# Optimization experiments

Measured on AMD Instinct MI355X. Metric: run time of the kernel, lower is better.

The kernel has to match this reference:

```python
import jax, jax.numpy as jnp
import numpy as np

V = 327696       # total nodes (4 graphs x 2 hemis x 40962 verts)
E = 1966080      # directed edges
C = 64           # feature dim
G = 4            # num graphs (subjects)
EPS = 1e-5


def setup_inputs() -> dict:
    key = jax.random.key(0)
    ks = jax.random.split(key, 10)
    x = jax.random.normal(ks[0], (V, C), dtype=jnp.float32)
    edge_index = jax.random.randint(ks[1], (2, E), 0, V, dtype=jnp.int64)
    batch = jnp.sort(jax.random.randint(ks[2], (V,), 0, G, dtype=jnp.int64))
    s = 1.0 / np.sqrt(C)
    return {
        "x": x,
        "edge_index": edge_index,
        "batch": batch,
        # GraphNorm 1 (PyG init: weight=1, bias=0, mean_scale=1)
        "norm1_w": jnp.ones((C,), jnp.float32),
        "norm1_b": jnp.zeros((C,), jnp.float32),
        "norm1_ms": jnp.ones((C,), jnp.float32),
        # SAGEConv linear layers: lin_l (on max-aggregated neighbors, with bias), lin_r (root, no bias)
        "lin_l_w": jax.random.uniform(ks[3], (C, C), jnp.float32, -s, s),
        "lin_l_b": jax.random.uniform(ks[4], (C,), jnp.float32, -s, s),
        "lin_r_w": jax.random.uniform(ks[5], (C, C), jnp.float32, -s, s),
        # GraphNorm 2
        "norm2_w": jnp.ones((C,), jnp.float32),
        "norm2_b": jnp.zeros((C,), jnp.float32),
        "norm2_ms": jnp.ones((C,), jnp.float32),
    }


def graph_norm(x, batch, weight, bias, mean_scale):
    # per-graph mean/var over nodes (PyG GraphNorm)
    ones = jnp.ones((x.shape[0], 1), x.dtype)
    cnt = jax.ops.segment_sum(ones, batch, num_segments=G)            # [G,1]
    mean = jax.ops.segment_sum(x, batch, num_segments=G) / cnt       # [G,C]
    centered = x - mean[batch] * mean_scale
    var = jax.ops.segment_sum(centered * centered, batch, num_segments=G) / cnt
    inv_std = jax.lax.rsqrt(var + EPS)
    return weight * centered * inv_std[batch] + bias


def sage_conv_max(x, edge_index, lin_l_w, lin_l_b, lin_r_w):
    src, dst = edge_index[0], edge_index[1]
    # scatter-max of source features onto destinations (irregular access)
    agg = jax.ops.segment_max(x[src], dst, num_segments=V)
    agg = jnp.where(jnp.isneginf(agg), 0.0, agg)  # nodes with no in-edges -> 0
    return agg @ lin_l_w + lin_l_b + x @ lin_r_w


def reference(x, edge_index, batch, norm1_w, norm1_b, norm1_ms,
              lin_l_w, lin_l_b, lin_r_w, norm2_w, norm2_b, norm2_ms):
    h = graph_norm(x, batch, norm1_w, norm1_b, norm1_ms)
    h = sage_conv_max(h, edge_index, lin_l_w, lin_l_b, lin_r_w)
    h = jax.nn.relu(x + h)
    h = graph_norm(h, batch, norm2_w, norm2_b, norm2_ms)
    return h
```

## Files before the change

kernel.cpp:

```cpp
#include <hip/hip_runtime.h>

#define V_NODES 327696
#define E_EDGES 1966080
#define C_DIM   64
#define G_NUM   4
#define EPS_GN  1e-5f
#define N_TILES (V_NODES/16)
#define SAGE_BLOCKS 2048
#define WAVES_TOTAL (SAGE_BLOCKS*4)
#define FILL_BLOCKS 512
#define H_BLOCKS 2048
#define NB_SCAN 1281
#define CH_SCAN2 6
#define PW 520
#define STAT_BLOCKS 2048
#define STAT_WAVES (STAT_BLOCKS*4)
#define TOTAL_F4 (V_NODES*16)
#define SW_CHUNK 640
#define HIST_BLOCKS 960

typedef short bf16x8 __attribute__((ext_vector_type(8)));
typedef float f32x4  __attribute__((ext_vector_type(4)));
typedef unsigned uintx4 __attribute__((ext_vector_type(4)));
typedef int intx4 __attribute__((ext_vector_type(4)));
typedef unsigned short u16x2 __attribute__((ext_vector_type(2)));

__device__ __forceinline__ unsigned short f2bf(float f) {
    unsigned u = __float_as_uint(f);
    return (unsigned short)((u + 0x7FFFu + ((u >> 16) & 1u)) >> 16);
}
__device__ __forceinline__ unsigned short encbf(float f) {
    unsigned short b = f2bf(f);
    return b ^ (unsigned short)(0x8000u | ((b >> 15) * 0x7FFFu));
}
__device__ __forceinline__ unsigned decp(unsigned e) {
    unsigned s = e & 0x80008000u;
    unsigned m = (s >> 15) * 0x7FFFu;
    return e ^ ~m;
}
__device__ __forceinline__ unsigned pkmaxu(unsigned a, unsigned b) {
    u16x2 xa = __builtin_bit_cast(u16x2, a);
    u16x2 xb = __builtin_bit_cast(u16x2, b);
    u16x2 r  = __builtin_elementwise_max(xa, xb);
    return __builtin_bit_cast(unsigned, r);
}

__global__ __launch_bounds__(256) void k_stats(const float* __restrict__ x,
                                               const int* __restrict__ batch,
                                               float* __restrict__ partial1) {
    __shared__ float red_s[256], red_q[256], red_c[G_NUM];
    const int t = threadIdx.x;
    red_s[t] = 0.0f; red_q[t] = 0.0f;
    if (t < G_NUM) red_c[t] = 0.0f;
    __syncthreads();

    const int w    = blockIdx.x * 4 + (t >> 6);
    const int lane = t & 63;
    const int base = w * SW_CHUNK;
    const int end  = (w == STAT_WAVES - 1) ? TOTAL_F4 : base + SW_CHUNK;
    const int c4   = (lane & 15) << 2;
    const bool cntr = (lane & 15) == 0;
    const float4* x4p = (const float4*)x;

    const int g0 = batch[base >> 4];
    const int g1 = batch[(end - 1) >> 4];

    if (g0 == g1 && end == base + SW_CHUNK) {
        float4 su = {0,0,0,0}, qu = {0,0,0,0};
        #pragma unroll
        for (int it = 0; it < 10; it++) {
            float4 v = x4p[base + lane + it * 64];
            su.x += v.x; su.y += v.y; su.z += v.z; su.w += v.w;
            qu.x = fmaf(v.x, v.x, qu.x); qu.y = fmaf(v.y, v.y, qu.y);
            qu.z = fmaf(v.z, v.z, qu.z); qu.w = fmaf(v.w, v.w, qu.w);
        }
        int p = (g0 << 6) + c4;
        atomicAdd(&red_s[p],   su.x); atomicAdd(&red_q[p],   qu.x);
        atomicAdd(&red_s[p+1], su.y); atomicAdd(&red_q[p+1], qu.y);
        atomicAdd(&red_s[p+2], su.z); atomicAdd(&red_q[p+2], qu.z);
        atomicAdd(&red_s[p+3], su.w); atomicAdd(&red_q[p+3], qu.w);
        if (cntr) atomicAdd(&red_c[g0], 10.0f);
    } else {
        for (int idx = base + lane; idx < end; idx += 64) {
            float4 v = x4p[idx];
            int g = batch[idx >> 4];
            int p = (g << 6) + c4;
            atomicAdd(&red_s[p],   v.x); atomicAdd(&red_q[p],   v.x * v.x);
            atomicAdd(&red_s[p+1], v.y); atomicAdd(&red_q[p+1], v.y * v.y);
            atomicAdd(&red_s[p+2], v.z); atomicAdd(&red_q[p+2], v.z * v.z);
            atomicAdd(&red_s[p+3], v.w); atomicAdd(&red_q[p+3], v.w * v.w);
            if (cntr) atomicAdd(&red_c[g], 1.0f);
        }
    }
    __syncthreads();
    float* row = partial1 + (size_t)blockIdx.x * PW;
    row[t] = red_s[t]; row[256 + t] = red_q[t];
    if (t < G_NUM) row[512 + t] = red_c[t];
}

__global__ __launch_bounds__(256) void k_hist(const int* __restrict__ ei,
                                              int* __restrict__ hist,
                                              unsigned short* __restrict__ rank) {
    const int t = blockIdx.x * 256 + threadIdx.x;
    const int* dst = ei + E_EDGES;
    const int e0 = t * 4;
    const int e1 = (E_EDGES / 2) + t * 4;
    intx4 a = *(const intx4*)(dst + e0);
    intx4 b = *(const intx4*)(dst + e1);
    int r0 = atomicAdd(&hist[a[0]], 1);
    int r1 = atomicAdd(&hist[a[1]], 1);
    int r2 = atomicAdd(&hist[a[2]], 1);
    int r3 = atomicAdd(&hist[a[3]], 1);
    int r4 = atomicAdd(&hist[b[0]], 1);
    int r5 = atomicAdd(&hist[b[1]], 1);
    int r6 = atomicAdd(&hist[b[2]], 1);
    int r7 = atomicAdd(&hist[b[3]], 1);
    ushort4 wa = { (unsigned short)r0, (unsigned short)r1,
                   (unsigned short)r2, (unsigned short)r3 };
    ushort4 wb = { (unsigned short)r4, (unsigned short)r5,
                   (unsigned short)r6, (unsigned short)r7 };
    *(ushort4*)(rank + e0) = wa;
    *(ushort4*)(rank + e1) = wb;
}

__global__ __launch_bounds__(256) void k_red(const float* __restrict__ partial,
                                             int nblocks, int nent,
                                             float* __restrict__ outs,
                                             float* __restrict__ outc) {
    int e = blockIdx.x * 4 + (threadIdx.x >> 6);
    int lane = threadIdx.x & 63;
    if (e >= nent) return;
    float s = 0.0f;
    for (int b = lane; b < nblocks; b += 64) s += partial[(size_t)b * PW + e];
    #pragma unroll
    for (int off = 1; off < 64; off <<= 1) s += __shfl_xor(s, off);
    if (lane == 0) { if (e < 512) outs[e] = s; else outc[e - 512] = s; }
}

__global__ __launch_bounds__(256) void k_scan1(const int* __restrict__ hist,
                                               int* __restrict__ bsum) {
    __shared__ int s[256];
    int i = blockIdx.x * 256 + threadIdx.x;
    s[threadIdx.x] = (i < V_NODES) ? hist[i] : 0;
    __syncthreads();
    for (int off = 128; off > 0; off >>= 1) {
        if (threadIdx.x < off) s[threadIdx.x] += s[threadIdx.x + off];
        __syncthreads();
    }
    if (threadIdx.x == 0) bsum[blockIdx.x] = s[0];
}

__global__ __launch_bounds__(256) void k_params(const float* __restrict__ sum,
                                                const float* __restrict__ sumsq,
                                                const float* __restrict__ cnt,
                                                const float* __restrict__ w,
                                                const float* __restrict__ b,
                                                const float* __restrict__ ms,
                                                float* __restrict__ scale,
                                                float* __restrict__ shift,
                                                const float* __restrict__ Wl,
                                                const float* __restrict__ Wr,
                                                char* __restrict__ gWsw,
                                                int do_wt,
                                                int* __restrict__ bsum) {
    if (blockIdx.x == 0) {
        int t = threadIdx.x;
        int g = t >> 6, c = t & 63;
        float n    = cnt[g];
        float mean = sum[t] / n;
        float msq  = sumsq[t] / n;
        float m    = ms[c];
        float var  = msq - 2.0f*m*mean*mean + m*m*mean*mean;
        float inv  = rsqrtf(var + EPS_GN);
        float sc   = w[c] * inv;
        scale[t] = sc;
        shift[t] = b[c] - mean * m * sc;
        if (do_wt) {
            for (int i = threadIdx.x; i < C_DIM*C_DIM; i += 256) {
                int k = i >> 6, col = i & 63;
                int boff = (col*128 + k*2) ^ ((col & 7) << 4);
                *(unsigned short*)(gWsw + boff)        = f2bf(Wl[i]);
                *(unsigned short*)(gWsw + 8192 + boff) = f2bf(Wr[i]);
            }
        }
    } else {
        __shared__ int s[256];
        int t = threadIdx.x;
        int loc[CH_SCAN2];
        int mysum = 0;
        #pragma unroll
        for (int j = 0; j < CH_SCAN2; j++) {
            int idx = t * CH_SCAN2 + j;
            loc[j] = (idx < NB_SCAN) ? bsum[idx] : 0;
            mysum += loc[j];
        }
        s[t] = mysum;
        __syncthreads();
        for (int off = 1; off < 256; off <<= 1) {
            int tmp = (t >= off) ? s[t - off] : 0;
            __syncthreads();
            s[t] += tmp;
            __syncthreads();
        }
        int ex = s[t] - mysum;
        #pragma unroll
        for (int j = 0; j < CH_SCAN2; j++) {
            int idx = t * CH_SCAN2 + j;
            if (idx < NB_SCAN) { bsum[idx] = ex; ex += loc[j]; }
        }
    }
}

__global__ __launch_bounds__(256) void k_scan3(const int* __restrict__ hist,
                                               const int* __restrict__ bsum,
                                               int* __restrict__ offs) {
    __shared__ int s[256];
    int t = threadIdx.x;
    int i = blockIdx.x * 256 + t;
    int v = (i < V_NODES) ? hist[i] : 0;
    s[t] = v;
    __syncthreads();
    for (int off = 1; off < 256; off <<= 1) {
        int tmp = (t >= off) ? s[t - off] : 0;
        __syncthreads();
        s[t] += tmp;
        __syncthreads();
    }
    int ex = s[t] - v + bsum[blockIdx.x];
    if (i < V_NODES) offs[i] = ex;
    if (i == 0) offs[V_NODES] = E_EDGES;
}

__global__ __launch_bounds__(256) void k_h_fill(const float* __restrict__ x,
                                                const int* __restrict__ batch,
                                                const float* __restrict__ scale1,
                                                const float* __restrict__ shift1,
                                                unsigned short* __restrict__ henc,
                                                const int* __restrict__ ei,
                                                const unsigned short* __restrict__ rank,
                                                const int* __restrict__ offs,
                                                int* __restrict__ slots) {
    if (blockIdx.x < FILL_BLOCKS) {
        int stride = FILL_BLOCKS * 256;
        for (int e = blockIdx.x * 256 + threadIdx.x; e < E_EDGES; e += stride) {
            int src = ei[e];
            int d   = ei[E_EDGES + e];
            slots[offs[d] + (int)rank[e]] = src;
        }
        return;
    }
    __shared__ float sc[256], sh[256];
    sc[threadIdx.x] = scale1[threadIdx.x];
    sh[threadIdx.x] = shift1[threadIdx.x];
    __syncthreads();
    const int total = V_NODES * 16;
    int bid = blockIdx.x - FILL_BLOCKS;
    int stride = H_BLOCKS * 256;
    const float4* x4 = (const float4*)x;
    ushort4* h4 = (ushort4*)henc;
    for (int i = bid * 256 + threadIdx.x; i < total; i += stride) {
        int v  = i >> 4;
        int c4 = (i & 15) << 2;
        int g  = batch[v];
        int p  = (g << 6) | c4;
        float4 val = x4[i];
        ushort4 o;
        o.x = encbf(fmaf(val.x, sc[p],   sh[p]));
        o.y = encbf(fmaf(val.y, sc[p+1], sh[p+1]));
        o.z = encbf(fmaf(val.z, sc[p+2], sh[p+2]));
        o.w = encbf(fmaf(val.w, sc[p+3], sh[p+3]));
        h4[i] = o;
    }
}

__global__ __launch_bounds__(256) void k_sage(const unsigned short* __restrict__ henc,
                                              const float* __restrict__ x,
                                              const int* __restrict__ batch,
                                              const int* __restrict__ offs,
                                              const int* __restrict__ slots,
                                              const char* __restrict__ gWsw,
                                              const float* __restrict__ bl,
                                              float* __restrict__ out,
                                              float* __restrict__ partial2) {
    __shared__ char lds_w[16384];
    __shared__ float red_s[256], red_q[256];
    {
        const float4* wsrc = (const float4*)gWsw;
        float4* wdst = (float4*)lds_w;
        for (int t = threadIdx.x; t < 1024; t += 256) wdst[t] = wsrc[t];
    }
    red_s[threadIdx.x] = 0.0f; red_q[threadIdx.x] = 0.0f;
    __syncthreads();

    const int lane = threadIdx.x & 63;
    const int wid  = threadIdx.x >> 6;
    const int lg = lane >> 4, lr = lane & 15;
    const char* hbase = (const char*)henc;

    float blv[4];
    #pragma unroll
    for (int cb = 0; cb < 4; cb++) blv[cb] = bl[cb*16 + lr];

    float su[4] = {0,0,0,0}, qu[4] = {0,0,0,0};
    int gc = -1;

    const int gwave = blockIdx.x * 4 + wid;
    for (int tile = gwave; tile < N_TILES; tile += WAVES_TOTAL) {
        const int rbase = tile << 4;
        const int myrow = rbase + lr;
        int st = offs[myrow];
        int en = offs[myrow + 1];

        const char* hr = hbase + ((unsigned)myrow << 7);
        uintx4 r0 = *(const uintx4*)(hr + lg*16);
        uintx4 r1 = *(const uintx4*)(hr + 64 + lg*16);

        uintx4 mA0 = {0,0,0,0}, mA1 = {0,0,0,0};
        uintx4 mB0 = {0,0,0,0}, mB1 = {0,0,0,0};
        for (int i = st & ~7; __ballot(i < en) != 0ull; i += 8) {
            intx4 qa = *(const intx4*)(slots + i);
            intx4 qb = *(const intx4*)(slots + i + 4);
            uintx4 a0[4], a1[4], b0[4], b1[4];
            #pragma unroll
            for (int e = 0; e < 4; e++) {
                int ia = i + e;
                unsigned idxa = (ia >= st && ia < en) ? (unsigned)qa[e] : (unsigned)V_NODES;
                const char* pa = hbase + (idxa << 7);
                a0[e] = *(const uintx4*)(pa + lg*16);
                a1[e] = *(const uintx4*)(pa + 64 + lg*16);
                int ib = i + 4 + e;
                unsigned idxb = (ib >= st && ib < en) ? (unsigned)qb[e] : (unsigned)V_NODES;
                const char* pb = hbase + (idxb << 7);
                b0[e] = *(const uintx4*)(pb + lg*16);
                b1[e] = *(const uintx4*)(pb + 64 + lg*16);
            }
            #pragma unroll
            for (int e = 0; e < 4; e++) {
                #pragma unroll
                for (int j = 0; j < 4; j++) {
                    mA0[j] = pkmaxu(mA0[j], a0[e][j]);
                    mA1[j] = pkmaxu(mA1[j], a1[e][j]);
                    mB0[j] = pkmaxu(mB0[j], b0[e][j]);
                    mB1[j] = pkmaxu(mB1[j], b1[e][j]);
                }
            }
        }
        bool has = en > st;
        uintx4 d0, d1;
        #pragma unroll
        for (int j = 0; j < 4; j++) {
            unsigned m0 = pkmaxu(mA0[j], mB0[j]);
            unsigned m1 = pkmaxu(mA1[j], mB1[j]);
            d0[j] = has ? decp(m0) : 0u;
            d1[j] = has ? decp(m1) : 0u;
            r0[j] = decp(r0[j]);
            r1[j] = decp(r1[j]);
        }
        bf16x8 a_agg0 = __builtin_bit_cast(bf16x8, d0);
        bf16x8 a_agg1 = __builtin_bit_cast(bf16x8, d1);
        bf16x8 a_h0   = __builtin_bit_cast(bf16x8, r0);
        bf16x8 a_h1   = __builtin_bit_cast(bf16x8, r1);

        f32x4 acc[4];
        #pragma unroll
        for (int cb = 0; cb < 4; cb++) {
            acc[cb] = (f32x4){0.f,0.f,0.f,0.f};
            int wrow = cb*16 + lr;
            int sw   = (wrow & 7) << 4;
            int o0   = (wrow*128 +      lg*16) ^ sw;
            int o1   = (wrow*128 + 64 + lg*16) ^ sw;
            bf16x8 wl0 = *(const bf16x8*)(lds_w + o0);
            bf16x8 wl1 = *(const bf16x8*)(lds_w + o1);
            bf16x8 wr0 = *(const bf16x8*)(lds_w + 8192 + o0);
            bf16x8 wr1 = *(const bf16x8*)(lds_w + 8192 + o1);
            acc[cb] = __builtin_amdgcn_mfma_f32_16x16x32_bf16(a_agg0, wl0, acc[cb], 0,0,0);
            acc[cb] = __builtin_amdgcn_mfma_f32_16x16x32_bf16(a_agg1, wl1, acc[cb], 0,0,0);
            acc[cb] = __builtin_amdgcn_mfma_f32_16x16x32_bf16(a_h0,   wr0, acc[cb], 0,0,0);
            acc[cb] = __builtin_amdgcn_mfma_f32_16x16x32_bf16(a_h1,   wr1, acc[cb], 0,0,0);
        }

        int g0 = batch[rbase], g15 = batch[rbase + 15];
        if (g0 == g15) {
            if (g0 != gc) {
                if (gc >= 0) {
                    #pragma unroll
                    for (int cb = 0; cb < 4; cb++) {
                        atomicAdd(&red_s[(gc<<6) + cb*16 + lr], su[cb]);
                        atomicAdd(&red_q[(gc<<6) + cb*16 + lr], qu[cb]);
                        su[cb] = 0.0f; qu[cb] = 0.0f;
                    }
                }
                gc = g0;
            }
            #pragma unroll
            for (int r = 0; r < 4; r++) {
                int row = rbase + lg*4 + r;
                #pragma unroll
                for (int cb = 0; cb < 4; cb++) {
                    int col = cb*16 + lr;
                    float xv = x[(size_t)row * C_DIM + col];
                    float o  = fmaxf(xv + acc[cb][r] + blv[cb], 0.0f);
                    out[(size_t)row * C_DIM + col] = o;
                    su[cb] += o; qu[cb] = fmaf(o, o, qu[cb]);
                }
            }
        } else {
            #pragma unroll
            for (int r = 0; r < 4; r++) {
                int row = rbase + lg*4 + r;
                int g   = batch[row];
                #pragma unroll
                for (int cb = 0; cb < 4; cb++) {
                    int col = cb*16 + lr;
                    float xv = x[(size_t)row * C_DIM + col];
                    float o  = fmaxf(xv + acc[cb][r] + blv[cb], 0.0f);
                    out[(size_t)row * C_DIM + col] = o;
                    int p = (g << 6) | col;
                    atomicAdd(&red_s[p], o);
                    atomicAdd(&red_q[p], o * o);
                }
            }
        }
    }
    if (gc >= 0) {
        #pragma unroll
        for (int cb = 0; cb < 4; cb++) {
            atomicAdd(&red_s[(gc<<6) + cb*16 + lr], su[cb]);
            atomicAdd(&red_q[(gc<<6) + cb*16 + lr], qu[cb]);
        }
    }
    __syncthreads();
    float* row = partial2 + (size_t)blockIdx.x * PW;
    row[threadIdx.x]       = red_s[threadIdx.x];
    row[256 + threadIdx.x] = red_q[threadIdx.x];
}

__global__ __launch_bounds__(256) void k_final(float* __restrict__ out,
                                               const int* __restrict__ batch,
                                               const float* __restrict__ scale2,
                                               const float* __restrict__ shift2) {
    __shared__ float sc[256], sh[256];
    sc[threadIdx.x] = scale2[threadIdx.x];
    sh[threadIdx.x] = shift2[threadIdx.x];
    __syncthreads();
    const int total = V_NODES * 16;
    int stride = gridDim.x * 256;
    float4* o4 = (float4*)out;
    for (int i = blockIdx.x * 256 + threadIdx.x; i < total; i += stride) {
        int v  = i >> 4;
        int c4 = (i & 15) << 2;
        int g  = batch[v];
        int p  = (g << 6) | c4;
        float4 val = o4[i];
        val.x = fmaf(val.x, sc[p],   sh[p]);
        val.y = fmaf(val.y, sc[p+1], sh[p+1]);
        val.z = fmaf(val.z, sc[p+2], sh[p+2]);
        val.w = fmaf(val.w, sc[p+3], sh[p+3]);
        o4[i] = val;
    }
}

extern "C" void kernel_launch(void* const* d_in, const int* in_sizes, int n_in,
                              void* d_out, int out_size, void* d_ws, size_t ws_size,
                              hipStream_t stream) {
    const float* x     = (const float*)d_in[0];
    const int*   ei    = (const int*)  d_in[1];
    const int*   batch = (const int*)  d_in[2];
    const float* n1w   = (const float*)d_in[3];
    const float* n1b   = (const float*)d_in[4];
    const float* n1ms  = (const float*)d_in[5];
    const float* Wl    = (const float*)d_in[6];
    const float* blv   = (const float*)d_in[7];
    const float* Wr    = (const float*)d_in[8];
    const float* n2w   = (const float*)d_in[9];
    const float* n2b   = (const float*)d_in[10];
    const float* n2ms  = (const float*)d_in[11];
    float* out = (float*)d_out;

    char* w = (char*)d_ws;
    unsigned short* henc = (unsigned short*)w; w += (size_t)(V_NODES + 1) * C_DIM * 2;
    int* slots           = (int*)w;            w += (size_t)E_EDGES * 4 + 64;
    int* hist            = (int*)w;            w += (size_t)V_NODES * 4;
    int* offs            = (int*)w;            w += (size_t)(V_NODES + 1) * 4 + 12;
    unsigned short* rank = (unsigned short*)w; w += (size_t)E_EDGES * 2;
    int* bsum            = (int*)w;            w += 1536 * 4;
    char* gWsw           = w;                  w += 16384;
    float* partial1      = (float*)w;          w += (size_t)STAT_BLOCKS * PW * 4;
    float* partial2      = (float*)w;          w += (size_t)SAGE_BLOCKS * PW * 4;
    float* stats  = (float*)w;
    float* sum1   = stats;
    float* sumsq1 = stats + 256;
    float* cnt    = stats + 512;
    float* sum2   = stats + 576;
    float* sumsq2 = stats + 832;
    float* scale1 = stats + 1088;
    float* shift1 = stats + 1344;
    float* scale2 = stats + 1600;
    float* shift2 = stats + 1856;

    hipMemsetAsync(hist, 0, (size_t)V_NODES * sizeof(int), stream);
    hipMemsetAsync(henc + (size_t)V_NODES * C_DIM, 0, C_DIM * 2, stream);

    k_stats <<<STAT_BLOCKS, 256, 0, stream>>>(x, batch, partial1);
    k_hist  <<<HIST_BLOCKS, 256, 0, stream>>>(ei, hist, rank);
    k_red   <<<129, 256, 0, stream>>>(partial1, STAT_BLOCKS, 516, sum1, cnt);
    k_scan1 <<<NB_SCAN, 256, 0, stream>>>(hist, bsum);
    k_params<<<2,   256, 0, stream>>>(sum1, sumsq1, cnt, n1w, n1b, n1ms,
                                      scale1, shift1, Wl, Wr, gWsw, 1, bsum);
    k_scan3 <<<NB_SCAN, 256, 0, stream>>>(hist, bsum, offs);
    k_h_fill<<<FILL_BLOCKS + H_BLOCKS, 256, 0, stream>>>(x, batch, scale1, shift1,
                                      henc, ei, rank, offs, slots);
    k_sage  <<<SAGE_BLOCKS, 256, 0, stream>>>(henc, x, batch, offs, slots,
                                      gWsw, blv, out, partial2);
    k_red   <<<128, 256, 0, stream>>>(partial2, SAGE_BLOCKS, 512, sum2, cnt);
    k_params<<<1,   256, 0, stream>>>(sum2, sumsq2, cnt, n2w, n2b, n2ms,
                                      scale2, shift2, (const float*)0, (const float*)0,
                                      (char*)0, 0, (int*)0);
    k_final <<<2048, 256, 0, stream>>>(out, batch, scale2, shift2);
}
```

Measured before the change: 358.6 us.

## Aggregate neighbor max per 16-row tile via LDS atomics and fuse small kernels

The scatter-max now walks one tile's contiguous edge range. Each lane fetches a 16-byte slice of a source row and applies LDS atomicMax into a per-wave staging buffer keyed by destination row. The destination row is packed into the high bits of the slot index. This replaces the per-row gather loop that wasted lanes on ragged degrees. Separately, the histogram and stats kernels are merged, the reduction and scan1 kernels are merged, and the second reduction is fused with param computation, cutting launch count. The trade is many LDS atomics plus per-tile zeroing and wave barriers, and it relies on node indices fitting in 27 bits.

New measurement: 363.5 us. About the same (+1.4%).

```diff
diff --git a/kernel.cpp b/kernel.cpp
--- a/kernel.cpp
+++ b/kernel.cpp
@@ -18,12 +18,14 @@
 #define TOTAL_F4 (V_NODES*16)
 #define SW_CHUNK 640
 #define HIST_BLOCKS 960
+#define RED_BLOCKS 129
+#define SROW 17
+#define STAGE_PAD 1280
 
 typedef short bf16x8 __attribute__((ext_vector_type(8)));
 typedef float f32x4  __attribute__((ext_vector_type(4)));
 typedef unsigned uintx4 __attribute__((ext_vector_type(4)));
 typedef int intx4 __attribute__((ext_vector_type(4)));
-typedef unsigned short u16x2 __attribute__((ext_vector_type(2)));
 
 __device__ __forceinline__ unsigned short f2bf(float f) {
     unsigned u = __float_as_uint(f);
@@ -38,33 +40,51 @@
     unsigned m = (s >> 15) * 0x7FFFu;
     return e ^ ~m;
 }
-__device__ __forceinline__ unsigned pkmaxu(unsigned a, unsigned b) {
-    u16x2 xa = __builtin_bit_cast(u16x2, a);
-    u16x2 xb = __builtin_bit_cast(u16x2, b);
-    u16x2 r  = __builtin_elementwise_max(xa, xb);
-    return __builtin_bit_cast(unsigned, r);
-}
-
-__global__ __launch_bounds__(256) void k_stats(const float* __restrict__ x,
-                                               const int* __restrict__ batch,
-                                               float* __restrict__ partial1) {
+
+__global__ __launch_bounds__(256) void k_pre(const float* __restrict__ x,
+                                             const int* __restrict__ batch,
+                                             const int* __restrict__ ei,
+                                             int* __restrict__ hist,
+                                             unsigned short* __restrict__ rank,
+                                             float* __restrict__ partial1) {
     __shared__ float red_s[256], red_q[256], red_c[G_NUM];
+    if (blockIdx.x < HIST_BLOCKS) {
+        const int t = blockIdx.x * 256 + threadIdx.x;
+        const int* dst = ei + E_EDGES;
+        const int e0 = t * 4;
+        const int e1 = (E_EDGES / 2) + t * 4;
+        intx4 a = *(const intx4*)(dst + e0);
+        intx4 b = *(const intx4*)(dst + e1);
+        int r0 = atomicAdd(&hist[a[0]], 1);
+        int r1 = atomicAdd(&hist[a[1]], 1);
+        int r2 = atomicAdd(&hist[a[2]], 1);
+        int r3 = atomicAdd(&hist[a[3]], 1);
+        int r4 = atomicAdd(&hist[b[0]], 1);
+        int r5 = atomicAdd(&hist[b[1]], 1);
+        int r6 = atomicAdd(&hist[b[2]], 1);
+        int r7 = atomicAdd(&hist[b[3]], 1);
+        ushort4 wa = { (unsigned short)r0, (unsigned short)r1,
+                       (unsigned short)r2, (unsigned short)r3 };
+        ushort4 wb = { (unsigned short)r4, (unsigned short)r5,
+                       (unsigned short)r6, (unsigned short)r7 };
+        *(ushort4*)(rank + e0) = wa;
+        *(ushort4*)(rank + e1) = wb;
+        return;
+    }
     const int t = threadIdx.x;
     red_s[t] = 0.0f; red_q[t] = 0.0f;
     if (t < G_NUM) red_c[t] = 0.0f;
     __syncthreads();
-
-    const int w    = blockIdx.x * 4 + (t >> 6);
+    const int bid  = blockIdx.x - HIST_BLOCKS;
+    const int w    = bid * 4 + (t >> 6);
     const int lane = t & 63;
     const int base = w * SW_CHUNK;
     const int end  = (w == STAT_WAVES - 1) ? TOTAL_F4 : base + SW_CHUNK;
     const int c4   = (lane & 15) << 2;
     const bool cntr = (lane & 15) == 0;
     const float4* x4p = (const float4*)x;
-
     const int g0 = batch[base >> 4];
     const int g1 = batch[(end - 1) >> 4];
-
     if (g0 == g1 && end == base + SW_CHUNK) {
         float4 su = {0,0,0,0}, qu = {0,0,0,0};
         #pragma unroll
@@ -93,61 +113,37 @@
         }
     }
     __syncthreads();
-    float* row = partial1 + (size_t)blockIdx.x * PW;
+    float* row = partial1 + (size_t)bid * PW;
     row[t] = red_s[t]; row[256 + t] = red_q[t];
     if (t < G_NUM) row[512 + t] = red_c[t];
 }
 
-__global__ __launch_bounds__(256) void k_hist(const int* __restrict__ ei,
-                                              int* __restrict__ hist,
-                                              unsigned short* __restrict__ rank) {
-    const int t = blockIdx.x * 256 + threadIdx.x;
-    const int* dst = ei + E_EDGES;
-    const int e0 = t * 4;
-    const int e1 = (E_EDGES / 2) + t * 4;
-    intx4 a = *(const intx4*)(dst + e0);
-    intx4 b = *(const intx4*)(dst + e1);
-    int r0 = atomicAdd(&hist[a[0]], 1);
-    int r1 = atomicAdd(&hist[a[1]], 1);
-    int r2 = atomicAdd(&hist[a[2]], 1);
-    int r3 = atomicAdd(&hist[a[3]], 1);
-    int r4 = atomicAdd(&hist[b[0]], 1);
-    int r5 = atomicAdd(&hist[b[1]], 1);
-    int r6 = atomicAdd(&hist[b[2]], 1);
-    int r7 = atomicAdd(&hist[b[3]], 1);
-    ushort4 wa = { (unsigned short)r0, (unsigned short)r1,
-                   (unsigned short)r2, (unsigned short)r3 };
-    ushort4 wb = { (unsigned short)r4, (unsigned short)r5,
-                   (unsigned short)r6, (unsigned short)r7 };
-    *(ushort4*)(rank + e0) = wa;
-    *(ushort4*)(rank + e1) = wb;
-}
-
-__global__ __launch_bounds__(256) void k_red(const float* __restrict__ partial,
-                                             int nblocks, int nent,
+__global__ __launch_bounds__(256) void k_rs1(const float* __restrict__ partial1,
+                                             const int* __restrict__ hist,
                                              float* __restrict__ outs,
-                                             float* __restrict__ outc) {
-    int e = blockIdx.x * 4 + (threadIdx.x >> 6);
-    int lane = threadIdx.x & 63;
-    if (e >= nent) return;
-    float s = 0.0f;
-    for (int b = lane; b < nblocks; b += 64) s += partial[(size_t)b * PW + e];
-    #pragma unroll
-    for (int off = 1; off < 64; off <<= 1) s += __shfl_xor(s, off);
-    if (lane == 0) { if (e < 512) outs[e] = s; else outc[e - 512] = s; }
-}
-
-__global__ __launch_bounds__(256) void k_scan1(const int* __restrict__ hist,
-                                               int* __restrict__ bsum) {
+                                             float* __restrict__ outc,
+                                             int* __restrict__ bsum) {
+    if (blockIdx.x < RED_BLOCKS) {
+        int e = blockIdx.x * 4 + (threadIdx.x >> 6);
+        int lane = threadIdx.x & 63;
+        if (e >= 516) return;
+        float s = 0.0f;
+        for (int b = lane; b < STAT_BLOCKS; b += 64) s += partial1[(size_t)b * PW + e];
+        #pragma unroll
+        for (int off = 1; off < 64; off <<= 1) s += __shfl_xor(s, off);
+        if (lane == 0) { if (e < 512) outs[e] = s; else outc[e - 512] = s; }
+        return;
+    }
     __shared__ int s[256];
-    int i = blockIdx.x * 256 + threadIdx.x;
+    int sb = blockIdx.x - RED_BLOCKS;
+    int i = sb * 256 + threadIdx.x;
     s[threadIdx.x] = (i < V_NODES) ? hist[i] : 0;
     __syncthreads();
     for (int off = 128; off > 0; off >>= 1) {
         if (threadIdx.x < off) s[threadIdx.x] += s[threadIdx.x + off];
         __syncthreads();
     }
-    if (threadIdx.x == 0) bsum[blockIdx.x] = s[0];
+    if (threadIdx.x == 0) bsum[sb] = s[0];
 }
 
 __global__ __launch_bounds__(256) void k_params(const float* __restrict__ sum,
@@ -161,7 +157,6 @@
                                                 const float* __restrict__ Wl,
                                                 const float* __restrict__ Wr,
                                                 char* __restrict__ gWsw,
-                                                int do_wt,
                                                 int* __restrict__ bsum) {
     if (blockIdx.x == 0) {
         int t = threadIdx.x;
@@ -175,13 +170,11 @@
         float sc   = w[c] * inv;
         scale[t] = sc;
         shift[t] = b[c] - mean * m * sc;
-        if (do_wt) {
-            for (int i = threadIdx.x; i < C_DIM*C_DIM; i += 256) {
-                int k = i >> 6, col = i & 63;
-                int boff = (col*128 + k*2) ^ ((col & 7) << 4);
-                *(unsigned short*)(gWsw + boff)        = f2bf(Wl[i]);
-                *(unsigned short*)(gWsw + 8192 + boff) = f2bf(Wr[i]);
-            }
+        for (int i = threadIdx.x; i < C_DIM*C_DIM; i += 256) {
+            int k = i >> 6, col = i & 63;
+            int boff = (col*128 + k*2) ^ ((col & 7) << 4);
+            *(unsigned short*)(gWsw + boff)        = f2bf(Wl[i]);
+            *(unsigned short*)(gWsw + 8192 + boff) = f2bf(Wr[i]);
         }
     } else {
         __shared__ int s[256];
@@ -245,7 +238,7 @@
         for (int e = blockIdx.x * 256 + threadIdx.x; e < E_EDGES; e += stride) {
             int src = ei[e];
             int d   = ei[E_EDGES + e];
-            slots[offs[d] + (int)rank[e]] = src;
+            slots[offs[d] + (int)rank[e]] = src | ((d & 15) << 27);
         }
         return;
     }
@@ -284,6 +277,7 @@
                                               float* __restrict__ partial2) {
     __shared__ char lds_w[16384];
     __shared__ float red_s[256], red_q[256];
+    __shared__ unsigned stage[4][STAGE_PAD];
     {
         const float4* wsrc = (const float4*)gWsw;
         float4* wdst = (float4*)lds_w;
@@ -295,7 +289,10 @@
     const int lane = threadIdx.x & 63;
     const int wid  = threadIdx.x >> 6;
     const int lg = lane >> 4, lr = lane & 15;
+    const int es = lane >> 3;
+    const int ss = lane & 7;
     const char* hbase = (const char*)henc;
+    unsigned* st_w = &stage[wid][0];
 
     float blv[4];
     #pragma unroll
@@ -307,52 +304,49 @@
     const int gwave = blockIdx.x * 4 + wid;
     for (int tile = gwave; tile < N_TILES; tile += WAVES_TOTAL) {
         const int rbase = tile << 4;
-        const int myrow = rbase + lr;
-        int st = offs[myrow];
-        int en = offs[myrow + 1];
-
-        const char* hr = hbase + ((unsigned)myrow << 7);
+        #pragma unroll
+        for (int z = 0; z < 5; z++)
+            *(uintx4*)(st_w + z*256 + lane*4) = (uintx4){0,0,0,0};
+        int o_lo = offs[rbase + lr];
+        int o_hi = offs[rbase + lr + 1];
+        bool has = o_hi > o_lo;
+        int st_t = __shfl(o_lo, 0);
+        int en_t = __shfl(o_hi, 15);
+        __builtin_amdgcn_wave_barrier();
+        for (int i = st_t; i < en_t; i += 8) {
+            int ii = i + es;
+            unsigned sv = (ii < en_t) ? (unsigned)slots[ii]
+                                      : (0x80000000u | (unsigned)V_NODES);
+            unsigned src = sv & 0x07FFFFFFu;
+            unsigned row = sv >> 27;
+            uintx4 hv = *(const uintx4*)(hbase + ((size_t)src << 7) + ss*16);
+            unsigned cb0 = (ss << 3);
+            #pragma unroll
+            for (int j = 0; j < 4; j++) {
+                atomicMax(&st_w[(cb0 + 2*j    ) * SROW + row], hv[j] & 0xFFFFu);
+                atomicMax(&st_w[(cb0 + 2*j + 1) * SROW + row], hv[j] >> 16);
+            }
+        }
+        __builtin_amdgcn_wave_barrier();
+        unsigned e0[8], e1[8];
+        #pragma unroll
+        for (int jj = 0; jj < 8; jj++) {
+            e0[jj] = st_w[(lg*8 + jj) * SROW + lr];
+            e1[jj] = st_w[(32 + lg*8 + jj) * SROW + lr];
+        }
+        __builtin_amdgcn_wave_barrier();
+        uintx4 d0, d1;
+        d0[0] = e0[0] | (e0[1] << 16); d0[1] = e0[2] | (e0[3] << 16);
+        d0[2] = e0[4] | (e0[5] << 16); d0[3] = e0[6] | (e0[7] << 16);
+        d1[0] = e1[0] | (e1[1] << 16); d1[1] = e1[2] | (e1[3] << 16);
+        d1[2] = e1[4] | (e1[5] << 16); d1[3] = e1[6] | (e1[7] << 16);
+        const char* hr = hbase + ((size_t)(rbase + lr) << 7);
         uintx4 r0 = *(const uintx4*)(hr + lg*16);
         uintx4 r1 = *(const uintx4*)(hr + 64 + lg*16);
-
-        uintx4 mA0 = {0,0,0,0}, mA1 = {0,0,0,0};
-        uintx4 mB0 = {0,0,0,0}, mB1 = {0,0,0,0};
-        for (int i = st & ~7; __ballot(i < en) != 0ull; i += 8) {
-            intx4 qa = *(const intx4*)(slots + i);
-            intx4 qb = *(const intx4*)(slots + i + 4);
-            uintx4 a0[4], a1[4], b0[4], b1[4];
-            #pragma unroll
-            for (int e = 0; e < 4; e++) {
-                int ia = i + e;
-                unsigned idxa = (ia >= st && ia < en) ? (unsigned)qa[e] : (unsigned)V_NODES;
-                const char* pa = hbase + (idxa << 7);
-                a0[e] = *(const uintx4*)(pa + lg*16);
-                a1[e] = *(const uintx4*)(pa + 64 + lg*16);
-                int ib = i + 4 + e;
-                unsigned idxb = (ib >= st && ib < en) ? (unsigned)qb[e] : (unsigned)V_NODES;
-                const char* pb = hbase + (idxb << 7);
-                b0[e] = *(const uintx4*)(pb + lg*16);
-                b1[e] = *(const uintx4*)(pb + 64 + lg*16);
-            }
-            #pragma unroll
-            for (int e = 0; e < 4; e++) {
-                #pragma unroll
-                for (int j = 0; j < 4; j++) {
-                    mA0[j] = pkmaxu(mA0[j], a0[e][j]);
-                    mA1[j] = pkmaxu(mA1[j], a1[e][j]);
-                    mB0[j] = pkmaxu(mB0[j], b0[e][j]);
-                    mB1[j] = pkmaxu(mB1[j], b1[e][j]);
-                }
-            }
-        }
-        bool has = en > st;
-        uintx4 d0, d1;
         #pragma unroll
         for (int j = 0; j < 4; j++) {
-            unsigned m0 = pkmaxu(mA0[j], mB0[j]);
-            unsigned m1 = pkmaxu(mA1[j], mB1[j]);
-            d0[j] = has ? decp(m0) : 0u;
-            d1[j] = has ? decp(m1) : 0u;
+            d0[j] = has ? decp(d0[j]) : 0u;
+            d1[j] = has ? decp(d1[j]) : 0u;
             r0[j] = decp(r0[j]);
             r1[j] = decp(r1[j]);
         }
@@ -435,6 +429,39 @@
     row[256 + threadIdx.x] = red_q[threadIdx.x];
 }
 
+__global__ __launch_bounds__(256) void k_red2p(const float* __restrict__ partial2,
+                                               const float* __restrict__ cnt,
+                                               const float* __restrict__ w,
+                                               const float* __restrict__ b,
+                                               const float* __restrict__ ms,
+                                               float* __restrict__ scale2,
+                                               float* __restrict__ shift2) {
+    int e = blockIdx.x * 4 + (threadIdx.x >> 6);
+    int lane = threadIdx.x & 63;
+    float s = 0.0f, q = 0.0f;
+    for (int bb = lane; bb < SAGE_BLOCKS; bb += 64) {
+        s += partial2[(size_t)bb * PW + e];
+        q += partial2[(size_t)bb * PW + 256 + e];
+    }
+    #pragma unroll
+    for (int off = 1; off < 64; off <<= 1) {
+        s += __shfl_xor(s, off);
+        q += __shfl_xor(q, off);
+    }
+    if (lane == 0) {
+        int g = e >> 6, c = e & 63;
+        float n    = cnt[g];
+        float mean = s / n;
+        float msq  = q / n;
+        float m    = ms[c];
+        float var  = msq - 2.0f*m*mean*mean + m*m*mean*mean;
+        float inv  = rsqrtf(var + EPS_GN);
+        float sc   = w[c] * inv;
+        scale2[e] = sc;
+        shift2[e] = b[c] - mean * m * sc;
+    }
+}
+
 __global__ __launch_bounds__(256) void k_final(float* __restrict__ out,
                                                const int* __restrict__ batch,
                                                const float* __restrict__ scale2,
@@ -491,30 +518,23 @@
     float* sum1   = stats;
     float* sumsq1 = stats + 256;
     float* cnt    = stats + 512;
-    float* sum2   = stats + 576;
-    float* sumsq2 = stats + 832;
-    float* scale1 = stats + 1088;
-    float* shift1 = stats + 1344;
-    float* scale2 = stats + 1600;
-    float* shift2 = stats + 1856;
+    float* scale1 = stats + 576;
+    float* shift1 = stats + 832;
+    float* scale2 = stats + 1088;
+    float* shift2 = stats + 1344;
 
     hipMemsetAsync(hist, 0, (size_t)V_NODES * sizeof(int), stream);
     hipMemsetAsync(henc + (size_t)V_NODES * C_DIM, 0, C_DIM * 2, stream);
 
-    k_stats <<<STAT_BLOCKS, 256, 0, stream>>>(x, batch, partial1);
-    k_hist  <<<HIST_BLOCKS, 256, 0, stream>>>(ei, hist, rank);
-    k_red   <<<129, 256, 0, stream>>>(partial1, STAT_BLOCKS, 516, sum1, cnt);
-    k_scan1 <<<NB_SCAN, 256, 0, stream>>>(hist, bsum);
-    k_params<<<2,   256, 0, stream>>>(sum1, sumsq1, cnt, n1w, n1b, n1ms,
-                                      scale1, shift1, Wl, Wr, gWsw, 1, bsum);
+    k_pre   <<<HIST_BLOCKS + STAT_BLOCKS, 256, 0, stream>>>(x, batch, ei, hist, rank, partial1);
+    k_rs1   <<<RED_BLOCKS + NB_SCAN, 256, 0, stream>>>(partial1, hist, sum1, cnt, bsum);
+    k_params<<<2,    256, 0, stream>>>(sum1, sumsq1, cnt, n1w, n1b, n1ms,
+                                       scale1, shift1, Wl, Wr, gWsw, bsum);
     k_scan3 <<<NB_SCAN, 256, 0, stream>>>(hist, bsum, offs);
     k_h_fill<<<FILL_BLOCKS + H_BLOCKS, 256, 0, stream>>>(x, batch, scale1, shift1,
-                                      henc, ei, rank, offs, slots);
+                                       henc, ei, rank, offs, slots);
     k_sage  <<<SAGE_BLOCKS, 256, 0, stream>>>(henc, x, batch, offs, slots,
-                                      gWsw, blv, out, partial2);
-    k_red   <<<128, 256, 0, stream>>>(partial2, SAGE_BLOCKS, 512, sum2, cnt);
-    k_params<<<1,   256, 0, stream>>>(sum2, sumsq2, cnt, n2w, n2b, n2ms,
-                                      scale2, shift2, (const float*)0, (const float*)0,
-                                      (char*)0, 0, (int*)0);
+                                       gWsw, blv, out, partial2);
+    k_red2p <<<64,   256, 0, stream>>>(partial2, cnt, n2w, n2b, n2ms, scale2, shift2);
     k_final <<<2048, 256, 0, stream>>>(out, batch, scale2, shift2);
 }
```
